# Kernel optimization log

Measured on AMD Instinct MI355X. Metric: run time of the kernel, lower is better.

Reference implementation:

```python
import jax, jax.numpy as jnp
import numpy as np
import math

DIM = 1024
H = 16
DK = DIM // H
SEG = 512
NN = 2      # num_neighbors
DIL = 4     # dilation
B, L = 2, 8192


def setup_inputs() -> dict:
    key = jax.random.key(0)
    ks = jax.random.split(key, 9)
    scale = 1.0 / math.sqrt(DIM)
    def lin(k):
        return jax.random.normal(k, (DIM, DIM), jnp.float32) * scale
    return {
        "x": jax.random.normal(ks[0], (B, L, DIM), jnp.float32),
        "Wq": lin(ks[1]), "bq": jnp.zeros((DIM,), jnp.float32),
        "Wk": lin(ks[2]), "bk": jnp.zeros((DIM,), jnp.float32),
        "Wv": lin(ks[3]), "bv": jnp.zeros((DIM,), jnp.float32),
        "Wo": lin(ks[4]), "bo": jnp.zeros((DIM,), jnp.float32),
    }


def _attn(q, k, v):
    # q: [B,S,H,Q,dk], k/v: [B,S,H,K,dk]
    scores = jnp.einsum('bshqd,bshkd->bshqk', q, k) / math.sqrt(q.shape[-1])
    a = jax.nn.softmax(scores, axis=-1)
    return jnp.einsum('bshqk,bshkd->bshqd', a, v)


def reference(x, Wq, bq, Wk, bk, Wv, bv, Wo, bo):
    Bx, Lx, C = x.shape
    pad = (-Lx) % SEG

    def proj_chunk(W, b):
        t = x @ W + b                                  # [B,L,C]
        t = jnp.pad(t, ((0, 0), (0, pad), (0, 0)))
        S = t.shape[1] // SEG
        t = t.reshape(Bx, S, SEG, H, DK)
        return t.transpose(0, 1, 3, 2, 4)              # [B,S,H,seg,dk]

    q = proj_chunk(Wq, bq)
    k = proj_chunk(Wk, bk)
    v = proj_chunk(Wv, bv)
    S = q.shape[1]

    # segment-local dense attention (vectorized over all segments)
    out = _attn(q, k, v)

    # dilated sampling of neighbor segments' keys/values
    dil_idx = jnp.arange(0, SEG, DIL)
    kd = k[:, :, :, dil_idx, :]                        # [B,S,H,seg/DIL,dk]
    vd = v[:, :, :, dil_idx, :]

    seg_ids = jnp.arange(S)
    w = 1.0 / (2 * NN)
    for off in range(1, NN + 1):
        for sign in (-1, 1):
            n = seg_ids + sign * off
            valid = (n >= 0) & (n < S)                 # [S]
            nc = jnp.clip(n, 0, S - 1)
            cross = _attn(q, kd[:, nc], vd[:, nc])     # [B,S,H,seg,dk]
            out = out + jnp.where(valid[None, :, None, None, None], cross * w, 0.0)

    out = out.transpose(0, 1, 3, 2, 4).reshape(Bx, S * SEG, C)
    out = out[:, :Lx, :]
    return out @ Wo + bo
```

## Files before the change

kernel.cpp:

```cpp
#include <hip/hip_runtime.h>
#include <stdint.h>

typedef __attribute__((ext_vector_type(8))) short short8;
typedef __attribute__((ext_vector_type(4))) float f32x4;

#define MFMA16(A_, B_, C_) __builtin_amdgcn_mfma_f32_16x16x32_bf16((A_), (B_), (C_), 0, 0, 0)

#if __has_builtin(__builtin_amdgcn_exp2f)
#define EXP2(x) __builtin_amdgcn_exp2f(x)
#else
#define EXP2(x) exp2f(x)
#endif

#define GLDS16(g_, l_)                                                        \
  __builtin_amdgcn_global_load_lds(                                           \
      (const __attribute__((address_space(1))) void*)(g_),                    \
      (__attribute__((address_space(3))) void*)(l_), 16, 0, 0)

__device__ __forceinline__ unsigned short f2bf(float f) {
  unsigned int u = __float_as_uint(f);
  u += 0x7fffu + ((u >> 16) & 1u);
  return (unsigned short)(u >> 16);
}

__device__ __forceinline__ unsigned pk2(float a, float b) {
  return (__float_as_uint(a) >> 16) | (__float_as_uint(b) & 0xffff0000u);
}


__global__ void cast_x_kernel(const float* __restrict__ x,
                              unsigned short* __restrict__ xb, int n4) {
  int i = blockIdx.x * blockDim.x + threadIdx.x;
  if (i >= n4) return;
  float4 v = reinterpret_cast<const float4*>(x)[i];
  uint2 pk;
  pk.x = (unsigned)f2bf(v.x) | ((unsigned)f2bf(v.y) << 16);
  pk.y = (unsigned)f2bf(v.z) | ((unsigned)f2bf(v.w) << 16);
  reinterpret_cast<uint2*>(xb)[i] = pk;
}

__global__ void transpose_cast4_kernel(const float* __restrict__ W0,
                                       const float* __restrict__ W1,
                                       const float* __restrict__ W2,
                                       const float* __restrict__ W3,
                                       unsigned short* __restrict__ T0,
                                       unsigned short* __restrict__ T1,
                                       unsigned short* __restrict__ T2,
                                       unsigned short* __restrict__ T3) {
  __shared__ float tile[32][33];
  const float* W = (blockIdx.z == 0) ? W0 : (blockIdx.z == 1) ? W1
                   : (blockIdx.z == 2) ? W2 : W3;
  unsigned short* Wt = (blockIdx.z == 0) ? T0 : (blockIdx.z == 1) ? T1
                       : (blockIdx.z == 2) ? T2 : T3;
  int k0 = blockIdx.x * 32, n0 = blockIdx.y * 32;
  int tx = threadIdx.x, ty = threadIdx.y;
  for (int i = ty; i < 32; i += 8)
    tile[i][tx] = W[(size_t)(k0 + i) * 1024 + n0 + tx];
  __syncthreads();
  for (int i = ty; i < 32; i += 8)
    Wt[(size_t)(n0 + i) * 1024 + k0 + tx] = f2bf(tile[tx][i]);
}

template<int MODE>
__global__ __launch_bounds__(512, 2) void gemm_kernel(
    const unsigned short* __restrict__ A,
    const unsigned short* __restrict__ W,
    const float* __restrict__ bias,
    unsigned short* __restrict__ out_bf,
    unsigned short* __restrict__ out_vtd,
    float* __restrict__ out_f) {
  __shared__ unsigned short Asm[2][256 * 64];
  __shared__ unsigned short Bsm[2][256 * 64];
  const int t = threadIdx.x;
  const int wg = (blockIdx.x & 7) * 32 + (blockIdx.x >> 3);
  const int m0 = (wg >> 2) * 256;
  const int n0 = (wg & 3) * 256;
  const int w = t >> 6, lane = t & 63, lr = lane & 15, lg = lane >> 4;
  const int wm = w >> 2, wn = w & 3;

  f32x4 acc[8][4];
#pragma unroll
  for (int i = 0; i < 8; ++i)
#pragma unroll
    for (int j = 0; j < 4; ++j) acc[i][j] = f32x4{0.f, 0.f, 0.f, 0.f};

  const int srow = lane >> 3;
  const int sswz = ((lane & 7) ^ srow) * 8;
  const int mrow = m0 + w * 32 + srow;
  const unsigned short* gA;
  size_t astep, arstride;
  if (MODE == 3) {
    gA = A + (size_t)(mrow >> 9) * (16 * 32768) + (size_t)(mrow & 511) * 64 + sswz;
    astep = 32768;
    arstride = 8 * 64;
  } else {
    gA = A + (size_t)mrow * 1024 + sswz;
    astep = 64;
    arstride = 8 * 1024;
  }
  const unsigned short* gB = W + (size_t)(n0 + w * 32 + srow) * 1024 + sswz;

  auto stage = [&](int buf, int kt) {
    const unsigned short* ga = gA + (size_t)kt * astep;
    const unsigned short* gb = gB + (size_t)kt * 64;
    unsigned short* la = &Asm[buf][(w * 32) * 64];
    unsigned short* lb = &Bsm[buf][(w * 32) * 64];
#pragma unroll
    for (int p = 0; p < 4; ++p) {
      GLDS16(ga + (size_t)p * arstride, la + p * 8 * 64);
      GLDS16(gb + (size_t)(p * 8) * 1024, lb + p * 8 * 64);
    }
  };

  const int rswz = (lr & 7);
  auto compute = [&](int buf) {
    const unsigned short* bA = &Asm[buf][0];
    const unsigned short* bB = &Bsm[buf][0];
    short8 bfv[2][4];
#pragma unroll
    for (int ks = 0; ks < 2; ++ks)
#pragma unroll
      for (int j = 0; j < 4; ++j) {
        const int row = wn * 64 + j * 16 + lr;
        bfv[ks][j] = *reinterpret_cast<const short8*>(
            &bB[row * 64 + (((ks * 4 + lg) ^ rswz) * 8)]);
      }
#pragma unroll
    for (int i = 0; i < 8; ++i) {
      const int row = wm * 128 + i * 16 + lr;
      short8 af[2];
#pragma unroll
      for (int ks = 0; ks < 2; ++ks)
        af[ks] = *reinterpret_cast<const short8*>(
            &bA[row * 64 + (((ks * 4 + lg) ^ rswz) * 8)]);
#pragma unroll
      for (int ks = 0; ks < 2; ++ks)
#pragma unroll
        for (int j = 0; j < 4; ++j)
          acc[i][j] = MFMA16(af[ks], bfv[ks][j], acc[i][j]);
    }
  };

  stage(0, 0);
#pragma unroll 1
  for (int kt = 0; kt < 15; ++kt) {
    stage((kt + 1) & 1, kt + 1);
    asm volatile("s_waitcnt vmcnt(8)\n\ts_barrier" ::: "memory");
    compute(kt & 1);
    asm volatile("s_waitcnt lgkmcnt(0)\n\ts_barrier" ::: "memory");
  }
  asm volatile("s_waitcnt vmcnt(0)\n\ts_barrier" ::: "memory");
  compute(1);

#pragma unroll
  for (int i = 0; i < 8; ++i)
#pragma unroll
    for (int j = 0; j < 4; ++j) {
      const int n = n0 + wn * 64 + j * 16 + lr;
      const float bv = bias[n];
#pragma unroll
      for (int r = 0; r < 4; ++r) {
        const int m = m0 + wm * 128 + i * 16 + lg * 4 + r;
        float val = acc[i][j][r] + bv;
        if (MODE == 3) {
          out_f[(size_t)m * 1024 + n] = val;
        } else {
          const int b = m >> 13, ll = m & 8191;
          const int ss = ll >> 9, rr = ll & 511;
          const int hh = n >> 6, d = n & 63;
          const size_t head = (size_t)((b * 16 + ss) * 16 + hh);
          if (MODE == 0) {
            out_bf[head * 32768 + rr * 64 + d] = f2bf(val * 0.18033688011112042f);
          } else if (MODE == 1) {
            out_bf[head * 32768 + rr * 64 + d] = f2bf(val);
          } else {
            const int p32 = (((rr >> 2) & 3) << 3) | (((rr >> 4) & 1) << 2) | (rr & 3);
            out_bf[head * 32768 + (size_t)d * 512 + ((rr & ~31) | p32)] = f2bf(val);
            if ((rr & 3) == 0) {
              const int cd = rr >> 2;
              const int pd = (((cd >> 2) & 3) << 3) | (((cd >> 4) & 1) << 2) | (cd & 3);
              out_vtd[head * 8192 + (size_t)d * 128 + ((cd & ~31) | pd)] = f2bf(val);
            }
          }
        }
      }
    }
}

__device__ __forceinline__ void attn_group(
    const unsigned short* __restrict__ Kp, int kstride,
    const unsigned short* __restrict__ Vp, int vstride,
    int nchunks, float wgt,
    const short8 (&qf)[4][2],
    unsigned short* __restrict__ Kl, unsigned short* __restrict__ Vl,
    f32x4 (&total)[4][4],
    int lr, int lg, int w, int lane) {
  const int srow = lane >> 3;
  const int fcw = (lane & 7) ^ srow;
  const unsigned short* gK = Kp + (size_t)(w * 8 + srow) * kstride + fcw * 8;
  const unsigned short* gV = Vp + (size_t)(w * 8 + srow) * vstride + fcw * 8;
  const int sx = lr & 7;

  float l[4] = {0.f, 0.f, 0.f, 0.f};
  f32x4 acc[4][4];
#pragma unroll
  for (int rt = 0; rt < 4; ++rt)
#pragma unroll
    for (int dt = 0; dt < 4; ++dt) acc[rt][dt] = f32x4{0.f, 0.f, 0.f, 0.f};

  GLDS16(gK, Kl + w * 512);
  GLDS16(gV, Vl + w * 512);
  __syncthreads();

  int cur = 0;
  for (int c = 0; c < nchunks; ++c) {
    if (c + 1 < nchunks) {
      GLDS16(gK + (size_t)((c + 1) * 64) * kstride, Kl + (cur ^ 1) * 4096 + w * 512);
      GLDS16(gV + (c + 1) * 64, Vl + (cur ^ 1) * 4096 + w * 512);
    }
    const unsigned short* bK = Kl + cur * 4096;
    const unsigned short* bV = Vl + cur * 4096;

#pragma unroll
    for (int kp = 0; kp < 2; ++kp) {
      short8 kf0[2], kf1[2], vf[4];
#pragma unroll
      for (int ks = 0; ks < 2; ++ks) {
        const int rc = (((ks * 4 + lg) ^ sx) * 8);
        kf0[ks] = *reinterpret_cast<const short8*>(&bK[(kp * 32 + lr) * 64 + rc]);
        kf1[ks] = *reinterpret_cast<const short8*>(&bK[(kp * 32 + 16 + lr) * 64 + rc]);
      }
      const int rcv = (((kp * 4 + lg) ^ sx) * 8);
#pragma unroll
      for (int dt = 0; dt < 4; ++dt)
        vf[dt] = *reinterpret_cast<const short8*>(&bV[(dt * 16 + lr) * 64 + rcv]);
#pragma unroll
      for (int rt = 0; rt < 4; ++rt) {
        f32x4 s0 = f32x4{0.f, 0.f, 0.f, 0.f};
        f32x4 s1 = f32x4{0.f, 0.f, 0.f, 0.f};
        __builtin_amdgcn_s_setprio(1);
#pragma unroll
        for (int ks = 0; ks < 2; ++ks) {
          s0 = MFMA16(kf0[ks], qf[rt][ks], s0);
          s1 = MFMA16(kf1[ks], qf[rt][ks], s1);
        }
        __builtin_amdgcn_s_setprio(0);
        float e0 = EXP2(s0[0]), e1 = EXP2(s0[1]), e2 = EXP2(s0[2]), e3 = EXP2(s0[3]);
        float e4 = EXP2(s1[0]), e5 = EXP2(s1[1]), e6 = EXP2(s1[2]), e7 = EXP2(s1[3]);
        l[rt] += ((e0 + e1) + (e2 + e3)) + ((e4 + e5) + (e6 + e7));
        uint4 wv;
        wv.x = pk2(e0, e1); wv.y = pk2(e2, e3);
        wv.z = pk2(e4, e5); wv.w = pk2(e6, e7);
        short8 pf = *reinterpret_cast<short8*>(&wv);
        __builtin_amdgcn_s_setprio(1);
#pragma unroll
        for (int dt = 0; dt < 4; ++dt)
          acc[rt][dt] = MFMA16(pf, vf[dt], acc[rt][dt]);
        __builtin_amdgcn_s_setprio(0);
      }
    }
    __syncthreads();
    cur ^= 1;
  }
#pragma unroll
  for (int rt = 0; rt < 4; ++rt) {
    float s = l[rt];
    s += __shfl_xor(s, 16);
    s += __shfl_xor(s, 32);
    float rl[4];
#pragma unroll
    for (int r = 0; r < 4; ++r) rl[r] = wgt / __shfl(s, lg * 4 + r);
#pragma unroll
    for (int dt = 0; dt < 4; ++dt)
#pragma unroll
      for (int r = 0; r < 4; ++r) total[rt][dt][r] += acc[rt][dt][r] * rl[r];
  }
}

__global__ __launch_bounds__(512, 2) void attn_kernel(
    const unsigned short* __restrict__ Q,
    const unsigned short* __restrict__ K,
    const unsigned short* __restrict__ Vt,
    const unsigned short* __restrict__ Vtd,
    unsigned short* __restrict__ AO) {
  __shared__ unsigned short Kl[2 * 4096];
  __shared__ unsigned short Vl[2 * 4096];
  const int bsh = blockIdx.x;
  const int h = bsh & 15, s = (bsh >> 4) & 15, b = bsh >> 8;
  const int t = threadIdx.x, w = t >> 6, lane = t & 63, lr = lane & 15, lg = lane >> 4;
  const int q0 = w * 64;

  const size_t headbase = (size_t)((b * 16 + s) * 16 + h);
  const unsigned short* Qp = Q + headbase * 32768 + (size_t)q0 * 64;
  short8 qf[4][2];
#pragma unroll
  for (int rt = 0; rt < 4; ++rt)
#pragma unroll
    for (int ks = 0; ks < 2; ++ks)
      qf[rt][ks] = *reinterpret_cast<const short8*>(&Qp[(rt * 16 + lr) * 64 + ks * 32 + lg * 8]);

  f32x4 total[4][4];
#pragma unroll
  for (int rt = 0; rt < 4; ++rt)
#pragma unroll
    for (int dt = 0; dt < 4; ++dt) total[rt][dt] = f32x4{0.f, 0.f, 0.f, 0.f};

  attn_group(K + headbase * 32768, 64, Vt + headbase * 32768, 512, 8, 1.0f,
             qf, Kl, Vl, total, lr, lg, w, lane);
#pragma unroll
  for (int gi = 0; gi < 4; ++gi) {
    const int off = (gi == 0) ? -2 : (gi == 1) ? -1 : (gi == 2) ? 1 : 2;
    const int ns = s + off;
    if (ns < 0 || ns > 15) continue;
    const size_t hb = (size_t)((b * 16 + ns) * 16 + h);
    attn_group(K + hb * 32768, 256, Vtd + hb * 8192, 128, 2, 0.25f,
               qf, Kl, Vl, total, lr, lg, w, lane);
  }
  const size_t obase = headbase * 32768 + (size_t)q0 * 64;
#pragma unroll
  for (int rt = 0; rt < 4; ++rt)
#pragma unroll
    for (int dt = 0; dt < 4; ++dt)
#pragma unroll
      for (int r = 0; r < 4; ++r) {
        const int q = rt * 16 + lg * 4 + r;
        const int d = dt * 16 + lr;
        AO[obase + (size_t)q * 64 + d] = f2bf(total[rt][dt][r]);
      }
}

extern "C" void kernel_launch(void* const* d_in, const int* in_sizes, int n_in,
                              void* d_out, int out_size, void* d_ws, size_t ws_size,
                              hipStream_t stream) {
  const float* x  = (const float*)d_in[0];
  const float* Wq = (const float*)d_in[1];
  const float* bq = (const float*)d_in[2];
  const float* Wk = (const float*)d_in[3];
  const float* bk = (const float*)d_in[4];
  const float* Wv = (const float*)d_in[5];
  const float* bv = (const float*)d_in[6];
  const float* Wo = (const float*)d_in[7];
  const float* bo = (const float*)d_in[8];
  float* out = (float*)d_out;

  char* ws = (char*)d_ws;
  unsigned short* Xb   = (unsigned short*)(ws);
  unsigned short* Wqt  = (unsigned short*)(ws + 33554432);
  unsigned short* Wkt  = (unsigned short*)(ws + 35651584);
  unsigned short* Wvt  = (unsigned short*)(ws + 37748736);
  unsigned short* Wot  = (unsigned short*)(ws + 39845888);
  unsigned short* Qb   = (unsigned short*)(ws + 41943040);
  unsigned short* Kb   = (unsigned short*)(ws + 75497472);
  unsigned short* Vtb  = (unsigned short*)(ws + 109051904);
  unsigned short* Vtdb = (unsigned short*)(ws + 142606336);
  unsigned short* AOb  = (unsigned short*)(ws + 150994944);

  cast_x_kernel<<<16384, 256, 0, stream>>>(x, Xb, 4194304);
  dim3 tb(32, 8), tg(32, 32, 4);
  transpose_cast4_kernel<<<tg, tb, 0, stream>>>(Wq, Wk, Wv, Wo, Wqt, Wkt, Wvt, Wot);

  gemm_kernel<0><<<256, 512, 0, stream>>>(Xb, Wqt, bq, Qb, nullptr, nullptr);
  gemm_kernel<1><<<256, 512, 0, stream>>>(Xb, Wkt, bk, Kb, nullptr, nullptr);
  gemm_kernel<2><<<256, 512, 0, stream>>>(Xb, Wvt, bv, Vtb, Vtdb, nullptr);

  attn_kernel<<<512, 512, 0, stream>>>(Qb, Kb, Vtb, Vtdb, AOb);

  gemm_kernel<3><<<256, 512, 0, stream>>>(AOb, Wot, bo, nullptr, nullptr, out);
}
```

Before: 311.5 us.

## Split attention query rows across two workgroups and restructure MFMA ordering

Each (b,s,h) segment's 512 queries are now split over two workgroups, so the grid doubles to 1024 blocks and each wave handles 32 query rows instead of 64. The inner loop is reordered so all QK^T MFMAs for both row tiles are issued first, followed by the PV MFMAs, with V fragments loaded just before use. The intent is more parallelism across the GPU's compute units and a lower per-wave register load. The cost is that every K/V tile is fetched from global into LDS twice as often, and the launch_bounds occupancy hint is dropped.

After: 287.4 us. 1.08x faster.

```diff
diff --git a/kernel.cpp b/kernel.cpp
--- a/kernel.cpp
+++ b/kernel.cpp
@@ -191,9 +191,9 @@
     const unsigned short* __restrict__ Kp, int kstride,
     const unsigned short* __restrict__ Vp, int vstride,
     int nchunks, float wgt,
-    const short8 (&qf)[4][2],
+    const short8 (&qf)[2][2],
     unsigned short* __restrict__ Kl, unsigned short* __restrict__ Vl,
-    f32x4 (&total)[4][4],
+    f32x4 (&total)[2][4],
     int lr, int lg, int w, int lane) {
   const int srow = lane >> 3;
   const int fcw = (lane & 7) ^ srow;
@@ -201,10 +201,10 @@
   const unsigned short* gV = Vp + (size_t)(w * 8 + srow) * vstride + fcw * 8;
   const int sx = lr & 7;
 
-  float l[4] = {0.f, 0.f, 0.f, 0.f};
-  f32x4 acc[4][4];
-#pragma unroll
-  for (int rt = 0; rt < 4; ++rt)
+  float l[2][2] = {{0.f, 0.f}, {0.f, 0.f}};
+  f32x4 acc[2][4];
+#pragma unroll
+  for (int rt = 0; rt < 2; ++rt)
 #pragma unroll
     for (int dt = 0; dt < 4; ++dt) acc[rt][dt] = f32x4{0.f, 0.f, 0.f, 0.f};
 
@@ -221,50 +221,60 @@
     const unsigned short* bK = Kl + cur * 4096;
     const unsigned short* bV = Vl + cur * 4096;
 
+    short8 pf[2][2];
 #pragma unroll
     for (int kp = 0; kp < 2; ++kp) {
-      short8 kf0[2], kf1[2], vf[4];
+      f32x4 s0[2], s1[2];
+#pragma unroll
+      for (int rt = 0; rt < 2; ++rt) {
+        s0[rt] = f32x4{0.f, 0.f, 0.f, 0.f};
+        s1[rt] = f32x4{0.f, 0.f, 0.f, 0.f};
+      }
+      __builtin_amdgcn_s_setprio(1);
 #pragma unroll
       for (int ks = 0; ks < 2; ++ks) {
         const int rc = (((ks * 4 + lg) ^ sx) * 8);
-        kf0[ks] = *reinterpret_cast<const short8*>(&bK[(kp * 32 + lr) * 64 + rc]);
-        kf1[ks] = *reinterpret_cast<const short8*>(&bK[(kp * 32 + 16 + lr) * 64 + rc]);
-      }
-      const int rcv = (((kp * 4 + lg) ^ sx) * 8);
-#pragma unroll
-      for (int dt = 0; dt < 4; ++dt)
-        vf[dt] = *reinterpret_cast<const short8*>(&bV[(dt * 16 + lr) * 64 + rcv]);
-#pragma unroll
-      for (int rt = 0; rt < 4; ++rt) {
-        f32x4 s0 = f32x4{0.f, 0.f, 0.f, 0.f};
-        f32x4 s1 = f32x4{0.f, 0.f, 0.f, 0.f};
-        __builtin_amdgcn_s_setprio(1);
-#pragma unroll
-        for (int ks = 0; ks < 2; ++ks) {
-          s0 = MFMA16(kf0[ks], qf[rt][ks], s0);
-          s1 = MFMA16(kf1[ks], qf[rt][ks], s1);
+        short8 kf0 = *reinterpret_cast<const short8*>(&bK[(kp * 32 + lr) * 64 + rc]);
+        short8 kf1 = *reinterpret_cast<const short8*>(&bK[(kp * 32 + 16 + lr) * 64 + rc]);
+#pragma unroll
+        for (int rt = 0; rt < 2; ++rt) {
+          s0[rt] = MFMA16(kf0, qf[rt][ks], s0[rt]);
+          s1[rt] = MFMA16(kf1, qf[rt][ks], s1[rt]);
         }
-        __builtin_amdgcn_s_setprio(0);
-        float e0 = EXP2(s0[0]), e1 = EXP2(s0[1]), e2 = EXP2(s0[2]), e3 = EXP2(s0[3]);
-        float e4 = EXP2(s1[0]), e5 = EXP2(s1[1]), e6 = EXP2(s1[2]), e7 = EXP2(s1[3]);
-        l[rt] += ((e0 + e1) + (e2 + e3)) + ((e4 + e5) + (e6 + e7));
+      }
+      __builtin_amdgcn_s_setprio(0);
+#pragma unroll
+      for (int rt = 0; rt < 2; ++rt) {
+        float e0 = EXP2(s0[rt][0]), e1 = EXP2(s0[rt][1]);
+        float e2 = EXP2(s0[rt][2]), e3 = EXP2(s0[rt][3]);
+        float e4 = EXP2(s1[rt][0]), e5 = EXP2(s1[rt][1]);
+        float e6 = EXP2(s1[rt][2]), e7 = EXP2(s1[rt][3]);
+        l[rt][kp] += ((e0 + e1) + (e2 + e3)) + ((e4 + e5) + (e6 + e7));
         uint4 wv;
         wv.x = pk2(e0, e1); wv.y = pk2(e2, e3);
         wv.z = pk2(e4, e5); wv.w = pk2(e6, e7);
-        short8 pf = *reinterpret_cast<short8*>(&wv);
-        __builtin_amdgcn_s_setprio(1);
-#pragma unroll
-        for (int dt = 0; dt < 4; ++dt)
-          acc[rt][dt] = MFMA16(pf, vf[dt], acc[rt][dt]);
-        __builtin_amdgcn_s_setprio(0);
-      }
-    }
+        pf[rt][kp] = *reinterpret_cast<short8*>(&wv);
+      }
+    }
+    __builtin_amdgcn_s_setprio(1);
+#pragma unroll
+    for (int ks = 0; ks < 2; ++ks) {
+      const int rcv = (((ks * 4 + lg) ^ sx) * 8);
+#pragma unroll
+      for (int dt = 0; dt < 4; ++dt) {
+        short8 vf = *reinterpret_cast<const short8*>(&bV[(dt * 16 + lr) * 64 + rcv]);
+#pragma unroll
+        for (int rt = 0; rt < 2; ++rt)
+          acc[rt][dt] = MFMA16(pf[rt][ks], vf, acc[rt][dt]);
+      }
+    }
+    __builtin_amdgcn_s_setprio(0);
     __syncthreads();
     cur ^= 1;
   }
 #pragma unroll
-  for (int rt = 0; rt < 4; ++rt) {
-    float s = l[rt];
+  for (int rt = 0; rt < 2; ++rt) {
+    float s = l[rt][0] + l[rt][1];
     s += __shfl_xor(s, 16);
     s += __shfl_xor(s, 32);
     float rl[4];
@@ -277,7 +287,7 @@
   }
 }
 
-__global__ __launch_bounds__(512, 2) void attn_kernel(
+__global__ __launch_bounds__(512) void attn_kernel(
     const unsigned short* __restrict__ Q,
     const unsigned short* __restrict__ K,
     const unsigned short* __restrict__ Vt,
@@ -285,23 +295,25 @@
     unsigned short* __restrict__ AO) {
   __shared__ unsigned short Kl[2 * 4096];
   __shared__ unsigned short Vl[2 * 4096];
-  const int bsh = blockIdx.x;
+  const int wg = blockIdx.x;
+  const int qh = wg & 1;
+  const int bsh = wg >> 1;
   const int h = bsh & 15, s = (bsh >> 4) & 15, b = bsh >> 8;
   const int t = threadIdx.x, w = t >> 6, lane = t & 63, lr = lane & 15, lg = lane >> 4;
-  const int q0 = w * 64;
+  const int q0 = qh * 256 + w * 32;
 
   const size_t headbase = (size_t)((b * 16 + s) * 16 + h);
   const unsigned short* Qp = Q + headbase * 32768 + (size_t)q0 * 64;
-  short8 qf[4][2];
-#pragma unroll
-  for (int rt = 0; rt < 4; ++rt)
+  short8 qf[2][2];
+#pragma unroll
+  for (int rt = 0; rt < 2; ++rt)
 #pragma unroll
     for (int ks = 0; ks < 2; ++ks)
       qf[rt][ks] = *reinterpret_cast<const short8*>(&Qp[(rt * 16 + lr) * 64 + ks * 32 + lg * 8]);
 
-  f32x4 total[4][4];
-#pragma unroll
-  for (int rt = 0; rt < 4; ++rt)
+  f32x4 total[2][4];
+#pragma unroll
+  for (int rt = 0; rt < 2; ++rt)
 #pragma unroll
     for (int dt = 0; dt < 4; ++dt) total[rt][dt] = f32x4{0.f, 0.f, 0.f, 0.f};
 
@@ -318,7 +330,7 @@
   }
   const size_t obase = headbase * 32768 + (size_t)q0 * 64;
 #pragma unroll
-  for (int rt = 0; rt < 4; ++rt)
+  for (int rt = 0; rt < 2; ++rt)
 #pragma unroll
     for (int dt = 0; dt < 4; ++dt)
 #pragma unroll
@@ -363,7 +375,7 @@
   gemm_kernel<1><<<256, 512, 0, stream>>>(Xb, Wkt, bk, Kb, nullptr, nullptr);
   gemm_kernel<2><<<256, 512, 0, stream>>>(Xb, Wvt, bv, Vtb, Vtdb, nullptr);
 
-  attn_kernel<<<512, 512, 0, stream>>>(Qb, Kb, Vtb, Vtdb, AOb);
+  attn_kernel<<<1024, 512, 0, stream>>>(Qb, Kb, Vtb, Vtdb, AOb);
 
   gemm_kernel<3><<<256, 512, 0, stream>>>(AOb, Wot, bo, nullptr, nullptr, out);
 }
```
